# Kernel tuning notes

Measured on AMD Instinct MI355X. Metric: run time of the kernel, lower is better.

## Reference

```python
import jax, jax.numpy as jnp
import numpy as np

N_EMBD = 2048
N_HEAD = 16
HEAD_DIM = N_EMBD // N_HEAD
LORA_R = 8
LORA_ALPHA = 1.0
LORA_SCALING = LORA_ALPHA / LORA_R


def setup_inputs() -> dict:
    key = jax.random.key(0)
    ks = jax.random.split(key, 10)
    B, T = 4, 2048
    init = LORA_ALPHA / LORA_R
    return {
        "x": jax.random.normal(ks[0], (B, T, N_EMBD), dtype=jnp.float32),
        "W_attn": jax.random.normal(ks[1], (N_EMBD, 3 * N_EMBD), dtype=jnp.float32) * 0.02,
        "b_attn": jnp.zeros((3 * N_EMBD,), dtype=jnp.float32),
        "lora_A_q": jax.random.normal(ks[2], (N_EMBD, LORA_R), dtype=jnp.float32) * init,
        "lora_B_q": jax.random.normal(ks[3], (LORA_R, N_EMBD), dtype=jnp.float32) * init,
        "lora_A_k": jax.random.normal(ks[4], (N_EMBD, LORA_R), dtype=jnp.float32) * init,
        "lora_B_k": jax.random.normal(ks[5], (LORA_R, N_EMBD), dtype=jnp.float32) * init,
        "W_proj": jax.random.normal(ks[6], (N_EMBD, N_EMBD), dtype=jnp.float32) * 0.02,
        "b_proj": jnp.zeros((N_EMBD,), dtype=jnp.float32),
    }


def _rotate_half(x):
    # torch: x1 = x[..., ::2]; x2 = x[..., 1::2]; cat((-x2, x1), -1)
    x1 = x[..., ::2]
    x2 = x[..., 1::2]
    return jnp.concatenate([-x2, x1], axis=-1)


def _rope_cos_sin(T, dtype):
    inv_freq = 1.0 / (10000.0 ** (jnp.arange(0, HEAD_DIM, 2, dtype=jnp.float32) / HEAD_DIM))
    t = jnp.arange(T, dtype=jnp.float32)
    freqs = jnp.einsum("i,j->ij", t, inv_freq)            # [T, D/2]
    emb = jnp.concatenate([freqs, freqs], axis=-1)          # [T, D]
    return jnp.cos(emb).astype(dtype), jnp.sin(emb).astype(dtype)


def reference(x, W_attn, b_attn, lora_A_q, lora_B_q, lora_A_k, lora_B_k, W_proj, b_proj):
    B, T, C = x.shape
    qkv = x @ W_attn + b_attn                                # [B,T,3C]
    q, k, v = jnp.split(qkv, 3, axis=2)
    # LoRA additions on q, k (applied to attn outputs, per module)
    q = q + (q @ lora_A_q) @ lora_B_q * LORA_SCALING
    k = k + (k @ lora_A_k) @ lora_B_k * LORA_SCALING

    def to_heads(z):
        return z.reshape(B, T, N_HEAD, HEAD_DIM).transpose(0, 2, 1, 3)  # [B,H,T,D]

    q, k, v = to_heads(q), to_heads(k), to_heads(v)
    cos, sin = _rope_cos_sin(T, x.dtype)                     # [T,D] each
    q = q * cos + _rotate_half(q) * sin
    k = k * cos + _rotate_half(k) * sin

    scale = 1.0 / jnp.sqrt(jnp.asarray(HEAD_DIM, dtype=x.dtype))
    scores = jnp.einsum("bhqd,bhkd->bhqk", q, k) * scale     # [B,H,T,T]
    causal = jnp.tril(jnp.ones((T, T), dtype=bool))
    scores = jnp.where(causal, scores, jnp.finfo(x.dtype).min)
    attn = jax.nn.softmax(scores, axis=-1)
    y = jnp.einsum("bhqk,bhkd->bhqd", attn, v)               # [B,H,T,D]
    y = y.transpose(0, 2, 1, 3).reshape(B, T, C)
    return y @ W_proj + b_proj
```

## Files before the change

### kernel.cpp

```cpp
#include <hip/hip_runtime.h>
#include <hip/hip_bf16.h>
#include <stdint.h>


typedef __attribute__((ext_vector_type(8))) short short8;
typedef __attribute__((ext_vector_type(4))) short short4v;
typedef __attribute__((ext_vector_type(4))) float floatx4;

#define EXP2F(x) __builtin_amdgcn_exp2f(x)

__device__ __forceinline__ float bf2f(short h) {
  union { unsigned int u; float f; } v;
  v.u = ((unsigned int)(unsigned short)h) << 16;
  return v.f;
}
__device__ __forceinline__ short f2bf(float f) {
  unsigned int u = __float_as_uint(f);
  unsigned int r = (u + 0x7FFFu + ((u >> 16) & 1u)) >> 16;
  return (short)r;
}
__device__ __forceinline__ short f2bf_n(float f) {
  __hip_bfloat16 h = __float2bfloat16(f);
  union { __hip_bfloat16 b; short s; } v; v.b = h; return v.s;
}

__device__ __forceinline__ void gload_lds16(const short* g, short* l) {
  __builtin_amdgcn_global_load_lds(
      (const __attribute__((address_space(1))) unsigned int*)g,
      (__attribute__((address_space(3))) unsigned int*)l, 16, 0, 0);
}

__device__ __forceinline__ void store_out(float* p, float v) { *p = v; }
__device__ __forceinline__ void store_out(short* p, float v) { *p = f2bf(v); }

__device__ __forceinline__ int xcd_swz(int orig, int nwg) {
  int q = nwg >> 3;
  return (orig & 7) * q + (orig >> 3);
}

#define SWZ(off, row) ((off) ^ (((row) & 7) << 3))

__global__ void k_f2b(const float* __restrict__ in, short* __restrict__ out, int n8) {
  int i = blockIdx.x * 256 + threadIdx.x;
  if (i >= n8) return;
  const float4* p = (const float4*)in + (size_t)i * 2;
  float4 a = p[0], b = p[1];
  short8 v;
  v[0] = f2bf(a.x); v[1] = f2bf(a.y); v[2] = f2bf(a.z); v[3] = f2bf(a.w);
  v[4] = f2bf(b.x); v[5] = f2bf(b.y); v[6] = f2bf(b.z); v[7] = f2bf(b.w);
  *(short8*)(out + (size_t)i * 8) = v;
}

__global__ void k_wT(const float* __restrict__ W, short* __restrict__ WT, int K, int N) {
  __shared__ float tile[32][33];
  int n0 = blockIdx.x * 32, k0 = blockIdx.y * 32;
  int tx = threadIdx.x, ty = threadIdx.y;
  #pragma unroll
  for (int i = 0; i < 4; i++)
    tile[ty + i * 8][tx] = W[(size_t)(k0 + ty + i * 8) * N + n0 + tx];
  __syncthreads();
  #pragma unroll
  for (int i = 0; i < 4; i++)
    WT[(size_t)(n0 + ty + i * 8) * K + k0 + tx] = f2bf(tile[tx][ty + i * 8]);
}

__global__ void k_ropetab(float* __restrict__ ct, float* __restrict__ st) {
  int t = blockIdx.x, j = threadIdx.x;
  float invf = powf(10000.0f, -(float)(2 * j) / 128.0f);
  float ang = (float)t * invf;
  ct[t * 64 + j] = cosf(ang);
  st[t * 64 + j] = sinf(ang);
}


#define GBAR __builtin_amdgcn_s_barrier();

#define RDA(QR) \
    _Pragma("unroll") for (int m_ = 0; m_ < 4; m_++) \
    _Pragma("unroll") for (int kk_ = 0; kk_ < 2; kk_++) { \
      int sA_ = ((QR) * 2 + wm) * 8192 + (m_ * 16 + c16) * 128 + kk_ * 64 + g * 16; \
      afr[m_][kk_] = *(const short8*)(Ab + ((sA_ ^ swzk) >> 1)); \
    }

#define RDBX(BB, QC, DST) \
    _Pragma("unroll") for (int n_ = 0; n_ < 2; n_++) \
    _Pragma("unroll") for (int kk_ = 0; kk_ < 2; kk_++) { \
      int sB_ = ((QC) * 4 + wn) * 4096 + (n_ * 16 + c16) * 128 + kk_ * 64 + g * 16; \
      DST[n_][kk_] = *(const short8*)((BB) + ((sB_ ^ swzk) >> 1)); \
    }

#define MM(QR, QC, BF) \
    __builtin_amdgcn_s_barrier(); \
    __builtin_amdgcn_s_setprio(1); \
    _Pragma("unroll") for (int kk_ = 0; kk_ < 2; kk_++) \
    _Pragma("unroll") for (int m_ = 0; m_ < 4; m_++) \
    _Pragma("unroll") for (int n_ = 0; n_ < 2; n_++) \
      acc[(QR) * 4 + m_][(QC) * 2 + n_] = __builtin_amdgcn_mfma_f32_16x16x32_bf16( \
          afr[m_][kk_], BF[n_][kk_], acc[(QR) * 4 + m_][(QC) * 2 + n_], 0, 0, 0); \
    __builtin_amdgcn_s_setprio(0);

template <typename OutT>
__global__ __launch_bounds__(512, 2) void k_gemm8(
    const short* __restrict__ A, const short* __restrict__ BT,
    const float* __restrict__ bias, OutT* __restrict__ C,
    int M, int N, int K)
{
  __shared__ __attribute__((aligned(16))) short lds[65536];
  const int tid = threadIdx.x;
  const int w = tid >> 6, l = tid & 63;
  const int g = l >> 4, c16 = l & 15;
  const int wm = w >> 2, wn = w & 3;
  const int swzk = (c16 & 7) << 4;

  const int nwg = gridDim.x * gridDim.y;
  const int wg = xcd_swz(blockIdx.y * gridDim.x + blockIdx.x, nwg);
  const int bm = wg % gridDim.x, bn = wg / gridDim.x;

  const short* Ablk = A + (size_t)bm * 256 * K;
  const short* Bblk = BT + (size_t)bn * 256 * K;

  floatx4 acc[8][4];
  #pragma unroll
  for (int i = 0; i < 8; i++)
    #pragma unroll
    for (int j = 0; j < 4; j++)
      acc[i][j] = (floatx4){0.f, 0.f, 0.f, 0.f};

  const int NT = K >> 6;
  const int L = NT >> 1;

  auto stageA = [&](int b, int h, int t) {
    short* dst = lds + b * 32768;
    int k0 = t * 64;
    #pragma unroll
    for (int j = 0; j < 2; j++) {
      int P = h * 2 + j;
      int sL = P * 8192 + tid * 16;
      int q = sL ^ (((sL >> 7) & 7) << 4);
      int row = (((((P & 1) << 1) | (P >> 1))) << 6) + ((sL >> 7) & 63);
      gload_lds16(Ablk + (size_t)row * K + k0 + ((q & 127) >> 1), dst + (sL >> 1));
    }
  };
  auto stageB = [&](int b, int h, int t) {
    short* dst = lds + b * 32768 + 16384;
    int k0 = t * 64;
    #pragma unroll
    for (int j = 0; j < 2; j++) {
      int sL = (h * 4 + 2 * j) * 4096 + tid * 16;
      int pos = sL >> 12;
      int q = sL ^ (((sL >> 7) & 7) << 4);
      int row = (((pos & 3) * 2 + (pos >> 2)) << 5) + ((sL >> 7) & 31);
      gload_lds16(Bblk + (size_t)row * K + k0 + ((q & 127) >> 1), dst + (sL >> 1));
    }
  };

  stageA(0, 0, 0); stageB(0, 0, 0); stageA(0, 1, 0); stageB(0, 1, 0);
  stageA(1, 0, 1); stageB(1, 0, 1); stageA(1, 1, 1); stageB(1, 1, 1);
  asm volatile("s_waitcnt vmcnt(8)" ::: "memory");
  __builtin_amdgcn_s_barrier();

  short8 bfr0[2][2], bfr1[2][2];
  RDBX(lds + 16384, 0, bfr0)

  #pragma unroll 1
  for (int i = 0; i < L; i++) {
    const int t2 = 2 * i + 2, t3 = 2 * i + 3;
    short8 afr[4][2];

    {
      const short* Ab = lds;
      RDA(0) if (i > 0) stageA(1, 1, 2 * i + 1);
      MM(0, 0, bfr0) GBAR
      RDBX(lds + 16384, 1, bfr1) if (t2 < NT) stageA(0, 0, t2);
      MM(0, 1, bfr1) GBAR
      RDA(1) if (t2 < NT) stageB(0, 0, t2);
      MM(1, 0, bfr0)
      if (t2 < NT) { asm volatile("s_waitcnt vmcnt(4)" ::: "memory"); }
      else         { asm volatile("s_waitcnt vmcnt(0)" ::: "memory"); }
      GBAR
      RDBX(lds + 49152, 0, bfr0) if (t2 < NT) stageB(0, 1, t2);
      MM(1, 1, bfr1) GBAR
    }
    {
      const short* Ab = lds + 32768;
      RDA(0) if (t2 < NT) stageA(0, 1, t2);
      MM(0, 0, bfr0) GBAR
      RDBX(lds + 49152, 1, bfr1) if (t3 < NT) stageA(1, 0, t3);
      MM(0, 1, bfr1) GBAR
      RDA(1) if (t3 < NT) stageB(1, 0, t3);
      MM(1, 0, bfr0)
      if (t3 < NT) { asm volatile("s_waitcnt vmcnt(4)" ::: "memory"); }
      else         { asm volatile("s_waitcnt vmcnt(0)" ::: "memory"); }
      GBAR
      if (t2 < NT) { RDBX(lds + 16384, 0, bfr0) }
      if (t3 < NT) stageB(1, 1, t3);
      MM(1, 1, bfr1) GBAR
    }
  }

  #pragma unroll
  for (int qr = 0; qr < 2; qr++)
    #pragma unroll
    for (int qc = 0; qc < 2; qc++)
      #pragma unroll
      for (int m = 0; m < 4; m++)
        #pragma unroll
        for (int n = 0; n < 2; n++) {
          int col = bn * 256 + wn * 64 + qc * 32 + n * 16 + c16;
          float bv = bias[col];
          #pragma unroll
          for (int r = 0; r < 4; r++) {
            size_t row = (size_t)bm * 256 + wm * 128 + qr * 64 + m * 16 + g * 4 + r;
            store_out(C + row * (size_t)N + col, acc[qr * 4 + m][qc * 2 + n][r] + bv);
          }
        }
}

__global__ __launch_bounds__(256, 2) void k_lorarope(
    short* __restrict__ qkv, const float* __restrict__ Aq, const float* __restrict__ Ak,
    const float* __restrict__ Bq, const float* __restrict__ Bk,
    const float* __restrict__ ct, const float* __restrict__ st)
{
  __shared__ float Bs[8 * 2048];
  __shared__ short Ls[2048];
  __shared__ float red[4][8];
  const int u = threadIdx.x;
  const int which = blockIdx.y;
  const float* Am = which ? Ak : Aq;
  const float* Bm = which ? Bk : Bq;
  const float qs = which ? 1.0f : 0.127517403f;

  #pragma unroll
  for (int i = 0; i < 16; i++) {
    int idx = (i * 256 + u) * 4;
    *(float4*)(Bs + idx) = *(const float4*)(Bm + idx);
  }
  float Areg[8][8];
  #pragma unroll
  for (int e = 0; e < 8; e++) {
    float4 a0 = *(const float4*)(Am + (size_t)(u * 8 + e) * 8);
    float4 a1 = *(const float4*)(Am + (size_t)(u * 8 + e) * 8 + 4);
    Areg[e][0] = a0.x; Areg[e][1] = a0.y; Areg[e][2] = a0.z; Areg[e][3] = a0.w;
    Areg[e][4] = a1.x; Areg[e][5] = a1.y; Areg[e][6] = a1.z; Areg[e][7] = a1.w;
  }
  __syncthreads();

  const int wv = u >> 6, l = u & 63;
  const int h = u >> 4, j0 = (u & 15) * 4;
  const int base = h * 128;
  const int t0 = blockIdx.x * 16;

  for (int tt = 0; tt < 16; tt++) {
    const int tok = t0 + tt;
    const int trow = tok & 2047;
    short* row = qkv + (size_t)tok * 6144 + which * 2048;

    __syncthreads();

    short8 q8 = *(const short8*)(row + u * 8);
    *(short8*)(Ls + u * 8) = q8;
    float part[8];
    #pragma unroll
    for (int r = 0; r < 8; r++) part[r] = 0.f;
    #pragma unroll
    for (int e = 0; e < 8; e++) {
      float qv = bf2f(q8[e]);
      #pragma unroll
      for (int r = 0; r < 8; r++) part[r] += qv * Areg[e][r];
    }
    #pragma unroll
    for (int r = 0; r < 8; r++)
      for (int off = 32; off > 0; off >>= 1)
        part[r] += __shfl_xor(part[r], off);
    if (l == 0) {
      #pragma unroll
      for (int r = 0; r < 8; r++) red[wv][r] = part[r];
    }
    __syncthreads();

    float Tr[8];
    #pragma unroll
    for (int r = 0; r < 8; r++)
      Tr[r] = (red[0][r] + red[1][r] + red[2][r] + red[3][r]) * 0.125f;

    float4 cv = *(const float4*)(ct + trow * 64 + j0);
    float4 sv = *(const float4*)(st + trow * 64 + j0);
    short4v qa4 = *(const short4v*)(Ls + base + j0);
    short4v qb4 = *(const short4v*)(Ls + base + 64 + j0);
    short8 qeo = *(const short8*)(Ls + base + 2 * j0);

    float o1[4], o2[4];
    #pragma unroll
    for (int j = 0; j < 4; j++) {
      float da = 0.f, db = 0.f, de = 0.f, dd = 0.f;
      #pragma unroll
      for (int r = 0; r < 8; r++) {
        const float* Br = Bs + r * 2048 + base;
        da += Tr[r] * Br[j0 + j];
        db += Tr[r] * Br[64 + j0 + j];
        de += Tr[r] * Br[2 * (j0 + j)];
        dd += Tr[r] * Br[2 * (j0 + j) + 1];
      }
      float qa = bf2f(qa4[j]) + da;
      float qb = bf2f(qb4[j]) + db;
      float qe = bf2f(qeo[2 * j]) + de;
      float qo = bf2f(qeo[2 * j + 1]) + dd;
      float c = ((const float*)&cv)[j], s = ((const float*)&sv)[j];
      o1[j] = (qa * c - qo * s) * qs;
      o2[j] = (qb * c + qe * s) * qs;
    }
    short4v w1, w2;
    #pragma unroll
    for (int j = 0; j < 4; j++) { w1[j] = f2bf(o1[j]); w2[j] = f2bf(o2[j]); }
    *(short4v*)(row + base + j0) = w1;
    *(short4v*)(row + base + 64 + j0) = w2;
  }
}

__global__ void k_vt(const short* __restrict__ qkv, short* __restrict__ vT) {
  __shared__ short tile[32][33];
  int bh = blockIdx.z, b = bh >> 4, h = bh & 15;
  int t0 = blockIdx.x * 32, d0 = blockIdx.y * 32;
  int tx = threadIdx.x, ty = threadIdx.y;
  #pragma unroll
  for (int i = 0; i < 4; i++) {
    int tt = t0 + ty + i * 8;
    tile[ty + i * 8][tx] = qkv[(size_t)(b * 2048 + tt) * 6144 + 4096 + h * 128 + d0 + tx];
  }
  __syncthreads();
  #pragma unroll
  for (int i = 0; i < 4; i++) {
    int d = d0 + ty + i * 8;
    vT[((size_t)bh * 128 + d) * 2048 + t0 + tx] = tile[tx][ty + i * 8];
  }
}

__global__ __launch_bounds__(256, 2) void k_attn(
    const short* __restrict__ qkv, const short* __restrict__ vT, short* __restrict__ y)
{
  __shared__ __attribute__((aligned(16))) short Ks[64 * 128];
  __shared__ __attribute__((aligned(16))) short Vs[128 * 64];
  __shared__ __attribute__((aligned(16))) short Ps[4 * 16 * 64];
  const int bh = blockIdx.x, b = bh >> 4, h = bh & 15;
  const int qt = 15 - (int)blockIdx.y;
  const int t = threadIdx.x, w = t >> 6, l = t & 63, g = l >> 4, c16 = l & 15;

  const int skr = t >> 2, sc0 = (t & 3) * 32;
  const int svd = t >> 1, sv0 = (t & 1) * 32;
  const short* kbase = qkv + (size_t)(b * 2048) * 6144 + 2048 + h * 128;
  const short* vbase = vT + (size_t)bh * 128 * 2048;
  short* Pw = Ps + w * (16 * 64);

  short8 onesv;
  #pragma unroll
  for (int e = 0; e < 8; e++) onesv[e] = (short)0x3F80;

  short8 qf[2][4];
  #pragma unroll
  for (int m = 0; m < 2; m++) {
    size_t goff = (size_t)(b * 2048 + qt * 128 + w * 32 + m * 16 + c16) * 6144 + h * 128;
    #pragma unroll
    for (int kf = 0; kf < 4; kf++)
      qf[m][kf] = *(const short8*)(qkv + goff + kf * 32 + 8 * g);
  }

  floatx4 o[2][8], ls[2];
  float mrow[2][4];
  #pragma unroll
  for (int m = 0; m < 2; m++) {
    #pragma unroll
    for (int nf = 0; nf < 8; nf++) o[m][nf] = (floatx4){0.f, 0.f, 0.f, 0.f};
    ls[m] = (floatx4){0.f, 0.f, 0.f, 0.f};
    #pragma unroll
    for (int r = 0; r < 4; r++) mrow[m][r] = -1e30f;
  }

  const int ntiles = 2 * qt + 2;

  short8 kreg[4], vreg[4];
  #pragma unroll
  for (int ii = 0; ii < 4; ii++) {
    kreg[ii] = *(const short8*)(kbase + (size_t)skr * 6144 + sc0 + ii * 8);
    vreg[ii] = *(const short8*)(vbase + (size_t)svd * 2048 + sv0 + ii * 8);
  }

  for (int kt = 0; kt < ntiles; kt++) {
    __syncthreads();
    #pragma unroll
    for (int ii = 0; ii < 4; ii++) {
      *(short8*)(Ks + SWZ(skr * 128 + sc0 + ii * 8, skr)) = kreg[ii];
      *(short8*)(Vs + SWZ(svd * 64 + sv0 + ii * 8, svd)) = vreg[ii];
    }
    __syncthreads();

    if (kt + 1 < ntiles) {
      #pragma unroll
      for (int ii = 0; ii < 4; ii++) {
        kreg[ii] = *(const short8*)(kbase + (size_t)((kt + 1) * 64 + skr) * 6144 + sc0 + ii * 8);
        vreg[ii] = *(const short8*)(vbase + (size_t)svd * 2048 + (kt + 1) * 64 + sv0 + ii * 8);
      }
    }

    floatx4 sc[2][4];
    #pragma unroll
    for (int m = 0; m < 2; m++)
      #pragma unroll
      for (int nf = 0; nf < 4; nf++) sc[m][nf] = (floatx4){0.f, 0.f, 0.f, 0.f};
    __builtin_amdgcn_s_setprio(1);
    #pragma unroll
    for (int kf = 0; kf < 4; kf++)
      #pragma unroll
      for (int nf = 0; nf < 4; nf++) {
        short8 kb = *(const short8*)(Ks + SWZ((nf * 16 + c16) * 128 + kf * 32 + 8 * g, c16));
        sc[0][nf] = __builtin_amdgcn_mfma_f32_16x16x32_bf16(qf[0][kf], kb, sc[0][nf], 0, 0, 0);
        sc[1][nf] = __builtin_amdgcn_mfma_f32_16x16x32_bf16(qf[1][kf], kb, sc[1][nf], 0, 0, 0);
      }
    __builtin_amdgcn_s_setprio(0);

    if (kt >= 2 * qt) {
      #pragma unroll
      for (int m = 0; m < 2; m++)
        #pragma unroll
        for (int nf = 0; nf < 4; nf++) {
          int key = kt * 64 + nf * 16 + c16;
          #pragma unroll
          for (int r = 0; r < 4; r++) {
            int qr = qt * 128 + w * 32 + m * 16 + g * 4 + r;
            if (key > qr) sc[m][nf][r] = -1e30f;
          }
        }
    }

    float need = -1e30f;
    #pragma unroll
    for (int m = 0; m < 2; m++)
      #pragma unroll
      for (int r = 0; r < 4; r++) {
        float rm = fmaxf(fmaxf(sc[m][0][r], sc[m][1][r]), fmaxf(sc[m][2][r], sc[m][3][r]));
        need = fmaxf(need, rm - mrow[m][r]);
      }
    if (!__all(need <= 11.0f)) {
      #pragma unroll
      for (int m = 0; m < 2; m++) {
        #pragma unroll
        for (int r = 0; r < 4; r++) {
          float rm = fmaxf(fmaxf(sc[m][0][r], sc[m][1][r]), fmaxf(sc[m][2][r], sc[m][3][r]));
          rm = fmaxf(rm, __shfl_xor(rm, 1));
          rm = fmaxf(rm, __shfl_xor(rm, 2));
          rm = fmaxf(rm, __shfl_xor(rm, 4));
          rm = fmaxf(rm, __shfl_xor(rm, 8));
          float mn = fmaxf(mrow[m][r], rm);
          float al = EXP2F(mrow[m][r] - mn);
          mrow[m][r] = mn;
          ls[m][r] *= al;
          #pragma unroll
          for (int nf = 0; nf < 8; nf++) o[m][nf][r] *= al;
        }
      }
    }

    short8 pa[2][2];
    #pragma unroll
    for (int m = 0; m < 2; m++) {
      #pragma unroll
      for (int r = 0; r < 4; r++) {
        int prow = g * 4 + r;
        #pragma unroll
        for (int nf = 0; nf < 4; nf++) {
          float p = EXP2F(sc[m][nf][r] - mrow[m][r]);
          Pw[SWZ(prow * 64 + nf * 16 + c16, prow)] = f2bf_n(p);
        }
      }
      #pragma unroll
      for (int kf = 0; kf < 2; kf++)
        pa[m][kf] = *(const short8*)(Pw + SWZ(c16 * 64 + kf * 32 + 8 * g, c16));
      if (m == 0) {
        asm volatile("s_waitcnt lgkmcnt(0)" ::: "memory");
        __builtin_amdgcn_sched_barrier(0);
      }
    }
    __builtin_amdgcn_s_setprio(1);
    #pragma unroll
    for (int m = 0; m < 2; m++)
      #pragma unroll
      for (int kf = 0; kf < 2; kf++)
        ls[m] = __builtin_amdgcn_mfma_f32_16x16x32_bf16(pa[m][kf], onesv, ls[m], 0, 0, 0);
    #pragma unroll
    for (int kf = 0; kf < 2; kf++)
      #pragma unroll
      for (int nf = 0; nf < 8; nf++) {
        short8 vb = *(const short8*)(Vs + SWZ((nf * 16 + c16) * 64 + kf * 32 + 8 * g, c16));
        o[0][nf] = __builtin_amdgcn_mfma_f32_16x16x32_bf16(pa[0][kf], vb, o[0][nf], 0, 0, 0);
        o[1][nf] = __builtin_amdgcn_mfma_f32_16x16x32_bf16(pa[1][kf], vb, o[1][nf], 0, 0, 0);
      }
    __builtin_amdgcn_s_setprio(0);
  }

  #pragma unroll
  for (int m = 0; m < 2; m++) {
    float ri[4];
    #pragma unroll
    for (int r = 0; r < 4; r++) ri[r] = 1.0f / ls[m][r];
    size_t yr0 = (size_t)(b * 2048 + qt * 128 + w * 32 + m * 16 + g * 4);
    #pragma unroll
    for (int nf = 0; nf < 8; nf++) {
      int col = h * 128 + nf * 16 + c16;
      #pragma unroll
      for (int r = 0; r < 4; r++)
        y[(yr0 + r) * 2048 + col] = f2bf_n(o[m][nf][r] * ri[r]);
    }
  }
}

extern "C" void kernel_launch(void* const* d_in, const int* in_sizes, int n_in,
                              void* d_out, int out_size, void* d_ws, size_t ws_size,
                              hipStream_t stream) {
  (void)in_sizes; (void)n_in; (void)out_size; (void)ws_size;
  const float* x      = (const float*)d_in[0];
  const float* W_attn = (const float*)d_in[1];
  const float* b_attn = (const float*)d_in[2];
  const float* Aq     = (const float*)d_in[3];
  const float* Bq     = (const float*)d_in[4];
  const float* Ak     = (const float*)d_in[5];
  const float* Bk     = (const float*)d_in[6];
  const float* W_proj = (const float*)d_in[7];
  const float* b_proj = (const float*)d_in[8];

  char* ws = (char*)d_ws;
  short* xb  = (short*)(ws + 0);
  short* WTa = (short*)(ws + 33554432);
  short* WTp = (short*)(ws + 58720256);
  short* qkv = (short*)(ws + 67108864);
  float* ct  = (float*)(ws + 168296448);
  float* st  = (float*)(ws + 168820736);
  short* vT  = (short*)(ws + 169345024);
  short* y   = xb;

  k_f2b<<<8192, 256, 0, stream>>>(x, xb, 2097152);
  k_wT<<<dim3(192, 64), dim3(32, 8), 0, stream>>>(W_attn, WTa, 2048, 6144);
  k_wT<<<dim3(64, 64), dim3(32, 8), 0, stream>>>(W_proj, WTp, 2048, 2048);
  k_ropetab<<<2048, 64, 0, stream>>>(ct, st);
  k_gemm8<short><<<dim3(32, 24), 512, 0, stream>>>(xb, WTa, b_attn, qkv, 8192, 6144, 2048);
  k_lorarope<<<dim3(512, 2), 256, 0, stream>>>(qkv, Aq, Ak, Bq, Bk, ct, st);
  k_vt<<<dim3(64, 4, 64), dim3(32, 8), 0, stream>>>(qkv, vT);
  k_attn<<<dim3(64, 16), 256, 0, stream>>>(qkv, vT, y);
  k_gemm8<float><<<dim3(32, 8), 512, 0, stream>>>(y, WTp, b_proj, (float*)d_out, 8192, 2048, 2048);
}
```

Measured before the change: 510.7 us.

## Replace 256x256 ping-pong GEMM with simpler 256x128 triple-buffered GEMM

```diff
diff --git a/kernel.cpp b/kernel.cpp
--- a/kernel.cpp
+++ b/kernel.cpp
@@ -72,148 +72,103 @@
   st[t * 64 + j] = sinf(ang);
 }
 
-
-#define GBAR __builtin_amdgcn_s_barrier();
-
-#define RDA(QR) \
-    _Pragma("unroll") for (int m_ = 0; m_ < 4; m_++) \
-    _Pragma("unroll") for (int kk_ = 0; kk_ < 2; kk_++) { \
-      int sA_ = ((QR) * 2 + wm) * 8192 + (m_ * 16 + c16) * 128 + kk_ * 64 + g * 16; \
-      afr[m_][kk_] = *(const short8*)(Ab + ((sA_ ^ swzk) >> 1)); \
-    }
-
-#define RDBX(BB, QC, DST) \
-    _Pragma("unroll") for (int n_ = 0; n_ < 2; n_++) \
-    _Pragma("unroll") for (int kk_ = 0; kk_ < 2; kk_++) { \
-      int sB_ = ((QC) * 4 + wn) * 4096 + (n_ * 16 + c16) * 128 + kk_ * 64 + g * 16; \
-      DST[n_][kk_] = *(const short8*)((BB) + ((sB_ ^ swzk) >> 1)); \
-    }
-
-#define MM(QR, QC, BF) \
-    __builtin_amdgcn_s_barrier(); \
-    __builtin_amdgcn_s_setprio(1); \
-    _Pragma("unroll") for (int kk_ = 0; kk_ < 2; kk_++) \
-    _Pragma("unroll") for (int m_ = 0; m_ < 4; m_++) \
-    _Pragma("unroll") for (int n_ = 0; n_ < 2; n_++) \
-      acc[(QR) * 4 + m_][(QC) * 2 + n_] = __builtin_amdgcn_mfma_f32_16x16x32_bf16( \
-          afr[m_][kk_], BF[n_][kk_], acc[(QR) * 4 + m_][(QC) * 2 + n_], 0, 0, 0); \
-    __builtin_amdgcn_s_setprio(0);
-
 template <typename OutT>
-__global__ __launch_bounds__(512, 2) void k_gemm8(
+__global__ __launch_bounds__(512, 1) void k_gemm3b(
     const short* __restrict__ A, const short* __restrict__ BT,
     const float* __restrict__ bias, OutT* __restrict__ C,
     int M, int N, int K)
 {
-  __shared__ __attribute__((aligned(16))) short lds[65536];
+  __shared__ __attribute__((aligned(16))) short lds[73728];
   const int tid = threadIdx.x;
   const int w = tid >> 6, l = tid & 63;
   const int g = l >> 4, c16 = l & 15;
-  const int wm = w >> 2, wn = w & 3;
-  const int swzk = (c16 & 7) << 4;
+  const int wm = w >> 1, wn = w & 1;
+  const int swzk = (c16 & 7) << 3;
 
   const int nwg = gridDim.x * gridDim.y;
   const int wg = xcd_swz(blockIdx.y * gridDim.x + blockIdx.x, nwg);
   const int bm = wg % gridDim.x, bn = wg / gridDim.x;
 
   const short* Ablk = A + (size_t)bm * 256 * K;
-  const short* Bblk = BT + (size_t)bn * 256 * K;
-
-  floatx4 acc[8][4];
-  #pragma unroll
-  for (int i = 0; i < 8; i++)
+  const short* Bblk = BT + (size_t)bn * 128 * K;
+
+  floatx4 acc[4][4];
+  #pragma unroll
+  for (int i = 0; i < 4; i++)
     #pragma unroll
     for (int j = 0; j < 4; j++)
       acc[i][j] = (floatx4){0.f, 0.f, 0.f, 0.f};
 
   const int NT = K >> 6;
-  const int L = NT >> 1;
-
-  auto stageA = [&](int b, int h, int t) {
-    short* dst = lds + b * 32768;
-    int k0 = t * 64;
-    #pragma unroll
-    for (int j = 0; j < 2; j++) {
-      int P = h * 2 + j;
-      int sL = P * 8192 + tid * 16;
-      int q = sL ^ (((sL >> 7) & 7) << 4);
-      int row = (((((P & 1) << 1) | (P >> 1))) << 6) + ((sL >> 7) & 63);
-      gload_lds16(Ablk + (size_t)row * K + k0 + ((q & 127) >> 1), dst + (sL >> 1));
-    }
+
+  auto stageA = [&](int buf, int j, int t) {
+    int sLs = j * 4096 + tid * 8;
+    int row = sLs >> 6;
+    int sc = ((tid & 7) ^ (row & 7)) * 8;
+    gload_lds16(Ablk + (size_t)row * K + t * 64 + sc, lds + buf * 16384 + sLs);
   };
-  auto stageB = [&](int b, int h, int t) {
-    short* dst = lds + b * 32768 + 16384;
-    int k0 = t * 64;
-    #pragma unroll
-    for (int j = 0; j < 2; j++) {
-      int sL = (h * 4 + 2 * j) * 4096 + tid * 16;
-      int pos = sL >> 12;
-      int q = sL ^ (((sL >> 7) & 7) << 4);
-      int row = (((pos & 3) * 2 + (pos >> 2)) << 5) + ((sL >> 7) & 31);
-      gload_lds16(Bblk + (size_t)row * K + k0 + ((q & 127) >> 1), dst + (sL >> 1));
-    }
+  auto stageB = [&](int buf, int j, int t) {
+    int sLs = j * 4096 + tid * 8;
+    int row = sLs >> 6;
+    int sc = ((tid & 7) ^ (row & 7)) * 8;
+    gload_lds16(Bblk + (size_t)row * K + t * 64 + sc, lds + 49152 + buf * 8192 + sLs);
   };
-
-  stageA(0, 0, 0); stageB(0, 0, 0); stageA(0, 1, 0); stageB(0, 1, 0);
-  stageA(1, 0, 1); stageB(1, 0, 1); stageA(1, 1, 1); stageB(1, 1, 1);
-  asm volatile("s_waitcnt vmcnt(8)" ::: "memory");
-  __builtin_amdgcn_s_barrier();
-
-  short8 bfr0[2][2], bfr1[2][2];
-  RDBX(lds + 16384, 0, bfr0)
+  auto stageTile = [&](int buf, int t) {
+    stageA(buf, 0, t); stageA(buf, 1, t); stageA(buf, 2, t); stageA(buf, 3, t);
+    stageB(buf, 0, t); stageB(buf, 1, t);
+  };
+
+  stageTile(0, 0); stageTile(1, 1);
 
   #pragma unroll 1
-  for (int i = 0; i < L; i++) {
-    const int t2 = 2 * i + 2, t3 = 2 * i + 3;
-    short8 afr[4][2];
-
-    {
-      const short* Ab = lds;
-      RDA(0) if (i > 0) stageA(1, 1, 2 * i + 1);
-      MM(0, 0, bfr0) GBAR
-      RDBX(lds + 16384, 1, bfr1) if (t2 < NT) stageA(0, 0, t2);
-      MM(0, 1, bfr1) GBAR
-      RDA(1) if (t2 < NT) stageB(0, 0, t2);
-      MM(1, 0, bfr0)
-      if (t2 < NT) { asm volatile("s_waitcnt vmcnt(4)" ::: "memory"); }
-      else         { asm volatile("s_waitcnt vmcnt(0)" ::: "memory"); }
-      GBAR
-      RDBX(lds + 49152, 0, bfr0) if (t2 < NT) stageB(0, 1, t2);
-      MM(1, 1, bfr1) GBAR
-    }
-    {
-      const short* Ab = lds + 32768;
-      RDA(0) if (t2 < NT) stageA(0, 1, t2);
-      MM(0, 0, bfr0) GBAR
-      RDBX(lds + 49152, 1, bfr1) if (t3 < NT) stageA(1, 0, t3);
-      MM(0, 1, bfr1) GBAR
-      RDA(1) if (t3 < NT) stageB(1, 0, t3);
-      MM(1, 0, bfr0)
-      if (t3 < NT) { asm volatile("s_waitcnt vmcnt(4)" ::: "memory"); }
-      else         { asm volatile("s_waitcnt vmcnt(0)" ::: "memory"); }
-      GBAR
-      if (t2 < NT) { RDBX(lds + 16384, 0, bfr0) }
-      if (t3 < NT) stageB(1, 1, t3);
-      MM(1, 1, bfr1) GBAR
-    }
-  }
-
-  #pragma unroll
-  for (int qr = 0; qr < 2; qr++)
-    #pragma unroll
-    for (int qc = 0; qc < 2; qc++)
+  for (int t = 0; t < NT; t++) {
+    if (t < NT - 2) { asm volatile("s_waitcnt vmcnt(6)" ::: "memory"); }
+    else            { asm volatile("s_waitcnt vmcnt(0)" ::: "memory"); }
+    __builtin_amdgcn_s_barrier();
+    const int buf = t % 3;
+    if (t + 2 < NT) stageTile((t + 2) % 3, t + 2);
+
+    const short* Ab = lds + buf * 16384;
+    const short* Bb = lds + 49152 + buf * 8192;
+    short8 afr[4][2], bfr[4][2];
+    #pragma unroll
+    for (int m = 0; m < 4; m++)
+      #pragma unroll
+      for (int kk = 0; kk < 2; kk++) {
+        int sA = (wm * 64 + m * 16 + c16) * 64 + kk * 32 + 8 * g;
+        afr[m][kk] = *(const short8*)(Ab + (sA ^ swzk));
+      }
+    #pragma unroll
+    for (int n = 0; n < 4; n++)
+      #pragma unroll
+      for (int kk = 0; kk < 2; kk++) {
+        int sB = (wn * 64 + n * 16 + c16) * 64 + kk * 32 + 8 * g;
+        bfr[n][kk] = *(const short8*)(Bb + (sB ^ swzk));
+      }
+    __builtin_amdgcn_s_setprio(1);
+    #pragma unroll
+    for (int kk = 0; kk < 2; kk++)
       #pragma unroll
       for (int m = 0; m < 4; m++)
         #pragma unroll
-        for (int n = 0; n < 2; n++) {
-          int col = bn * 256 + wn * 64 + qc * 32 + n * 16 + c16;
-          float bv = bias[col];
-          #pragma unroll
-          for (int r = 0; r < 4; r++) {
-            size_t row = (size_t)bm * 256 + wm * 128 + qr * 64 + m * 16 + g * 4 + r;
-            store_out(C + row * (size_t)N + col, acc[qr * 4 + m][qc * 2 + n][r] + bv);
-          }
-        }
+        for (int n = 0; n < 4; n++)
+          acc[m][n] = __builtin_amdgcn_mfma_f32_16x16x32_bf16(
+              afr[m][kk], bfr[n][kk], acc[m][n], 0, 0, 0);
+    __builtin_amdgcn_s_setprio(0);
+  }
+
+  #pragma unroll
+  for (int m = 0; m < 4; m++)
+    #pragma unroll
+    for (int n = 0; n < 4; n++) {
+      int col = bn * 128 + wn * 64 + n * 16 + c16;
+      float bv = bias[col];
+      #pragma unroll
+      for (int r = 0; r < 4; r++) {
+        size_t row = (size_t)bm * 256 + wm * 64 + m * 16 + g * 4 + r;
+        store_out(C + row * (size_t)N + col, acc[m][n][r] + bv);
+      }
+    }
 }
 
 __global__ __launch_bounds__(256, 2) void k_lorarope(
@@ -540,9 +495,9 @@
   k_wT<<<dim3(192, 64), dim3(32, 8), 0, stream>>>(W_attn, WTa, 2048, 6144);
   k_wT<<<dim3(64, 64), dim3(32, 8), 0, stream>>>(W_proj, WTp, 2048, 2048);
   k_ropetab<<<2048, 64, 0, stream>>>(ct, st);
-  k_gemm8<short><<<dim3(32, 24), 512, 0, stream>>>(xb, WTa, b_attn, qkv, 8192, 6144, 2048);
+  k_gemm3b<short><<<dim3(32, 48), 512, 0, stream>>>(xb, WTa, b_attn, qkv, 8192, 6144, 2048);
   k_lorarope<<<dim3(512, 2), 256, 0, stream>>>(qkv, Aq, Ak, Bq, Bk, ct, st);
   k_vt<<<dim3(64, 4, 64), dim3(32, 8), 0, stream>>>(qkv, vT);
   k_attn<<<dim3(64, 16), 256, 0, stream>>>(qkv, vT, y);
-  k_gemm8<float><<<dim3(32, 8), 512, 0, stream>>>(y, WTp, b_proj, (float*)d_out, 8192, 2048, 2048);
-}
+  k_gemm3b<float><<<dim3(32, 16), 512, 0, stream>>>(y, WTp, b_proj, (float*)d_out, 8192, 2048, 2048);
+}
```

Result: slower. 604.0 us (median of 2 runs) (+18.3%).

## Fuse V transpose into QKV GEMM epilogue, drop separate transpose kernel

Applied to the files above, without the earlier changes.

```diff
diff --git a/kernel.cpp b/kernel.cpp
--- a/kernel.cpp
+++ b/kernel.cpp
@@ -100,12 +100,12 @@
     __builtin_amdgcn_s_setprio(0);
 
 template <typename OutT>
-__global__ __launch_bounds__(512, 2) void k_gemm8(
+__global__ __launch_bounds__(512, 1) void k_gemm8(
     const short* __restrict__ A, const short* __restrict__ BT,
     const float* __restrict__ bias, OutT* __restrict__ C,
-    int M, int N, int K)
+    int M, int N, int K, short* __restrict__ vTo)
 {
-  __shared__ __attribute__((aligned(16))) short lds[65536];
+  __shared__ __attribute__((aligned(16))) short lds[66048];
   const int tid = threadIdx.x;
   const int w = tid >> 6, l = tid & 63;
   const int g = l >> 4, c16 = l & 15;
@@ -198,6 +198,36 @@
     }
   }
 
+  if (vTo && bn >= 16) {
+    #pragma unroll
+    for (int qr = 0; qr < 2; qr++)
+      #pragma unroll
+      for (int qc = 0; qc < 2; qc++)
+        #pragma unroll
+        for (int m = 0; m < 4; m++)
+          #pragma unroll
+          for (int n = 0; n < 2; n++) {
+            int dl = wn * 64 + qc * 32 + n * 16 + c16;
+            float bv = bias[bn * 256 + dl];
+            #pragma unroll
+            for (int r = 0; r < 4; r++) {
+              int tl = wm * 128 + qr * 64 + m * 16 + g * 4 + r;
+              lds[dl * 258 + tl] = f2bf_n(acc[qr * 4 + m][qc * 2 + n][r] + bv);
+            }
+          }
+    __syncthreads();
+    const int dl = tid >> 1, th = (tid & 1) * 128;
+    const int col = bn * 256 + dl;
+    const int hh = (col - 4096) >> 7, dd = col & 127;
+    const int bb = bm >> 3, tt0 = (bm & 7) * 256 + th;
+    short* dst = vTo + ((size_t)((bb * 16 + hh) * 128 + dd)) * 2048 + tt0;
+    const short* src = lds + dl * 258 + th;
+    #pragma unroll
+    for (int i2 = 0; i2 < 16; i2++)
+      *(short8*)(dst + i2 * 8) = *(const short8*)(src + i2 * 8);
+    return;
+  }
+
   #pragma unroll
   for (int qr = 0; qr < 2; qr++)
     #pragma unroll
@@ -314,24 +344,6 @@
     for (int j = 0; j < 4; j++) { w1[j] = f2bf(o1[j]); w2[j] = f2bf(o2[j]); }
     *(short4v*)(row + base + j0) = w1;
     *(short4v*)(row + base + 64 + j0) = w2;
-  }
-}
-
-__global__ void k_vt(const short* __restrict__ qkv, short* __restrict__ vT) {
-  __shared__ short tile[32][33];
-  int bh = blockIdx.z, b = bh >> 4, h = bh & 15;
-  int t0 = blockIdx.x * 32, d0 = blockIdx.y * 32;
-  int tx = threadIdx.x, ty = threadIdx.y;
-  #pragma unroll
-  for (int i = 0; i < 4; i++) {
-    int tt = t0 + ty + i * 8;
-    tile[ty + i * 8][tx] = qkv[(size_t)(b * 2048 + tt) * 6144 + 4096 + h * 128 + d0 + tx];
-  }
-  __syncthreads();
-  #pragma unroll
-  for (int i = 0; i < 4; i++) {
-    int d = d0 + ty + i * 8;
-    vT[((size_t)bh * 128 + d) * 2048 + t0 + tx] = tile[tx][ty + i * 8];
   }
 }
 
@@ -540,9 +552,8 @@
   k_wT<<<dim3(192, 64), dim3(32, 8), 0, stream>>>(W_attn, WTa, 2048, 6144);
   k_wT<<<dim3(64, 64), dim3(32, 8), 0, stream>>>(W_proj, WTp, 2048, 2048);
   k_ropetab<<<2048, 64, 0, stream>>>(ct, st);
-  k_gemm8<short><<<dim3(32, 24), 512, 0, stream>>>(xb, WTa, b_attn, qkv, 8192, 6144, 2048);
+  k_gemm8<short><<<dim3(32, 24), 512, 0, stream>>>(xb, WTa, b_attn, qkv, 8192, 6144, 2048, vT);
   k_lorarope<<<dim3(512, 2), 256, 0, stream>>>(qkv, Aq, Ak, Bq, Bk, ct, st);
-  k_vt<<<dim3(64, 4, 64), dim3(32, 8), 0, stream>>>(qkv, vT);
   k_attn<<<dim3(64, 16), 256, 0, stream>>>(qkv, vT, y);
-  k_gemm8<float><<<dim3(32, 8), 512, 0, stream>>>(y, WTp, b_proj, (float*)d_out, 8192, 2048, 2048);
-}
+  k_gemm8<float><<<dim3(32, 8), 512, 0, stream>>>(y, WTp, b_proj, (float*)d_out, 8192, 2048, 2048, nullptr);
+}
```

Measured after the change: 512.7 us. Within noise of the previous version (+0.4%).
